# Optimization experiments

Hardware: AMD Instinct MI355X
Metric: run time of the kernel (lower is better)

Reference implementation:

```python
import jax, jax.numpy as jnp
import numpy as np

SHAPES = ((16, 16), (32, 32), (64, 64), (128, 128))  # (H, W) per level, low-res first
IN_CH = (2048, 1024, 512, 256)
B = 2; D = 256; HEADS = 4; PTS = 4; NLVL = 4; NLAYER = 3; DH = D // HEADS; FFN = 1024
LQ = sum(h * w for h, w in SHAPES)  # 21760


def _group_norm(x, g, b, groups=32, eps=1e-5):
    Bn, C, H, W = x.shape
    xr = x.reshape(Bn, groups, C // groups, H, W)
    m = xr.mean((2, 3, 4), keepdims=True)
    v = xr.var((2, 3, 4), keepdims=True)
    xr = (xr - m) / jnp.sqrt(v + eps)
    return xr.reshape(Bn, C, H, W) * g[None, :, None, None] + b[None, :, None, None]


def _layer_norm(x, g, b, eps=1e-5):
    m = x.mean(-1, keepdims=True)
    v = x.var(-1, keepdims=True)
    return (x - m) / jnp.sqrt(v + eps) * g + b


def _sine_pos(H, W):
    # PositionEmbeddingSine(num_pos_feats=D//2, normalize=True), mask all-valid
    nh = D // 2
    scale = 2.0 * np.pi
    dim_t = (10000.0 ** (2.0 * (jnp.arange(nh) // 2) / nh)).astype(jnp.float32)
    def enc(n, e):
        p = e[:, None] / dim_t  # (n, nh)
        return jnp.stack([jnp.sin(p[:, 0::2]), jnp.cos(p[:, 1::2])], -1).reshape(n, nh)
    ye = (jnp.arange(1, H + 1, dtype=jnp.float32) / (H + 1e-6)) * scale
    xe = (jnp.arange(1, W + 1, dtype=jnp.float32) / (W + 1e-6)) * scale
    py = enc(H, ye)  # (H, nh)
    px = enc(W, xe)  # (W, nh)
    pos = jnp.concatenate([jnp.broadcast_to(py[:, None], (H, W, nh)),
                           jnp.broadcast_to(px[None, :], (H, W, nh))], -1)
    return pos.reshape(H * W, D)


def _ref_points():
    refs = []
    for H, W in SHAPES:
        ry = (jnp.arange(H, dtype=jnp.float32) + 0.5) / H
        rx = (jnp.arange(W, dtype=jnp.float32) + 0.5) / W
        gy, gx = jnp.meshgrid(ry, rx, indexing='ij')
        refs.append(jnp.stack([gx.reshape(-1), gy.reshape(-1)], -1))
    return jnp.concatenate(refs, 0)  # (LQ, 2) in (x, y), identical across levels (valid_ratios==1)


def _bilinear(v, loc, H, W):
    # v: (B, HEADS, H*W, DH); loc: (B, LQ, HEADS, PTS, 2) normalized in [0,1]
    # grid_sample align_corners=False semantics: pixel = loc*size - 0.5, zero padding
    x = (loc[..., 0] * W - 0.5).transpose(0, 2, 1, 3)  # (B, HEADS, LQ, PTS)
    y = (loc[..., 1] * H - 0.5).transpose(0, 2, 1, 3)
    x0f = jnp.floor(x); y0f = jnp.floor(y)
    tx = x - x0f; ty = y - y0f
    x0 = x0f.astype(jnp.int32); y0 = y0f.astype(jnp.int32)
    def g(yi, xi):
        valid = ((xi >= 0) & (xi < W) & (yi >= 0) & (yi < H)).astype(v.dtype)
        idx = jnp.clip(yi, 0, H - 1) * W + jnp.clip(xi, 0, W - 1)
        out = jnp.take_along_axis(v, idx.reshape(B, HEADS, -1)[..., None], axis=2)
        return out.reshape(B, HEADS, LQ, PTS, DH) * valid[..., None]
    w00 = (1 - ty) * (1 - tx); w01 = (1 - ty) * tx
    w10 = ty * (1 - tx); w11 = ty * tx
    return (g(y0, x0) * w00[..., None] + g(y0, x0 + 1) * w01[..., None]
            + g(y0 + 1, x0) * w10[..., None] + g(y0 + 1, x0 + 1) * w11[..., None])


def _model(xs, pws, pbs, ggs, gbs, level_embed, Woff, boff, Wattn, battn,
           Wval, bval, Wout, bout, ng, nb, W1, b1, W2, b2):
    srcs, poss = [], []
    for i, ((H, W), x, pw, pb, gg, gb) in enumerate(zip(SHAPES, xs, pws, pbs, ggs, gbs)):
        z = jnp.einsum('bchw,dc->bdhw', x, pw) + pb[None, :, None, None]  # 1x1 conv
        z = _group_norm(z, gg, gb)
        srcs.append(z.reshape(B, D, H * W).transpose(0, 2, 1))  # (B, HW, D)
        poss.append(_sine_pos(H, W)[None] + level_embed[i][None, None])
    src = jnp.concatenate(srcs, 1)   # (B, LQ, D)
    pos = jnp.concatenate(poss, 1)   # (1, LQ, D)
    refs = _ref_points()             # (LQ, 2)
    wh = jnp.array([(W, H) for H, W in SHAPES], jnp.float32)  # (NLVL, 2) (x=W, y=H)
    for l in range(NLAYER):
        q = src + pos
        off = (q @ Woff[l] + boff[l]).reshape(B, LQ, HEADS, NLVL, PTS, 2)
        aw = jax.nn.softmax((q @ Wattn[l] + battn[l]).reshape(B, LQ, HEADS, NLVL * PTS), -1)
        aw = aw.reshape(B, LQ, HEADS, NLVL, PTS)
        val = (src @ Wval[l] + bval[l]).reshape(B, LQ, HEADS, DH)
        loc = refs[None, :, None, None, None, :] + off / wh[None, None, None, :, None, :]
        out = jnp.zeros((B, HEADS, LQ, DH), src.dtype)
        start = 0
        for lv, (H, W) in enumerate(SHAPES):
            n = H * W
            v = val[:, start:start + n].transpose(0, 2, 1, 3)        # (B, HEADS, n, DH)
            samp = _bilinear(v, loc[:, :, :, lv], H, W)              # (B, HEADS, LQ, PTS, DH)
            w = aw[:, :, :, lv].transpose(0, 2, 1, 3)                # (B, HEADS, LQ, PTS)
            out = out + jnp.einsum('bhqpd,bhqp->bhqd', samp, w)
            start += n
        attn_out = out.transpose(0, 2, 1, 3).reshape(B, LQ, D) @ Wout[l] + bout[l]
        src = _layer_norm(src + attn_out, ng[l], nb[l])
        # NOTE: per source, MLP output replaces src (no second residual)
        src = jax.nn.relu(src @ W1[l] + b1[l]) @ W2[l] + b2[l]
    return src


def setup_inputs():
    key = jax.random.key(0)
    ks = iter(jax.random.split(key, 24))
    inp = {}
    for i, (c, (H, W)) in enumerate(zip(IN_CH, SHAPES)):
        inp[f'x{i}'] = jax.random.normal(next(ks), (B, c, H, W), jnp.float32)
        inp[f'pw{i}'] = jax.random.normal(next(ks), (D, c), jnp.float32) / np.float32(np.sqrt(c))
        inp[f'pb{i}'] = jnp.zeros((D,), jnp.float32)
        inp[f'gg{i}'] = jnp.ones((D,), jnp.float32)
        inp[f'gb{i}'] = jnp.zeros((D,), jnp.float32)
    inp['level_embed'] = jax.random.normal(next(ks), (NLVL, D), jnp.float32)
    inp['Woff'] = jax.random.normal(next(ks), (NLAYER, D, HEADS * NLVL * PTS * 2), jnp.float32) * 0.01
    inp['boff'] = jax.random.normal(next(ks), (NLAYER, HEADS * NLVL * PTS * 2), jnp.float32) * 0.5
    inp['Wattn'] = jax.random.normal(next(ks), (NLAYER, D, HEADS * NLVL * PTS), jnp.float32) * 0.01
    inp['battn'] = jnp.zeros((NLAYER, HEADS * NLVL * PTS), jnp.float32)
    inp['Wval'] = jax.random.normal(next(ks), (NLAYER, D, D), jnp.float32) / 16.0
    inp['bval'] = jnp.zeros((NLAYER, D), jnp.float32)
    inp['Wout'] = jax.random.normal(next(ks), (NLAYER, D, D), jnp.float32) / 16.0
    inp['bout'] = jnp.zeros((NLAYER, D), jnp.float32)
    inp['ng'] = jnp.ones((NLAYER, D), jnp.float32)
    inp['nb'] = jnp.zeros((NLAYER, D), jnp.float32)
    inp['W1'] = jax.random.normal(next(ks), (NLAYER, D, FFN), jnp.float32) / 16.0
    inp['b1'] = jnp.zeros((NLAYER, FFN), jnp.float32)
    inp['W2'] = jax.random.normal(next(ks), (NLAYER, FFN, D), jnp.float32) / 32.0
    inp['b2'] = jnp.zeros((NLAYER, D), jnp.float32)
    return inp


def reference(x0, pw0, pb0, gg0, gb0, x1, pw1, pb1, gg1, gb1,
              x2, pw2, pb2, gg2, gb2, x3, pw3, pb3, gg3, gb3,
              level_embed, Woff, boff, Wattn, battn, Wval, bval, Wout, bout,
              ng, nb, W1, b1, W2, b2):
    return _model((x0, x1, x2, x3), (pw0, pw1, pw2, pw3), (pb0, pb1, pb2, pb3),
                  (gg0, gg1, gg2, gg3), (gb0, gb1, gb2, gb3), level_embed,
                  Woff, boff, Wattn, battn, Wval, bval, Wout, bout,
                  ng, nb, W1, b1, W2, b2)
```

## Files before the change

kernel.cpp:

```cpp
#include <hip/hip_runtime.h>
#include <math.h>

#define LQ 21760
#define NB 2

typedef __attribute__((ext_vector_type(8))) short bf16x8;
typedef __attribute__((ext_vector_type(4))) float f32x4;

static __device__ __forceinline__ float wave_sum(float v) {
#pragma unroll
    for (int o = 32; o > 0; o >>= 1) v += __shfl_down(v, o, 64);
    return v;
}

static __device__ __forceinline__ unsigned short f2bf(float f) {
    unsigned int u = __float_as_uint(f);
    u = (u + 0x7fffu + ((u >> 16) & 1u)) >> 16;
    return (unsigned short)u;
}
static __device__ __forceinline__ float bf2f(unsigned short h) {
    return __uint_as_float((unsigned int)h << 16);
}

__global__ __launch_bounds__(256) void zero_buf(float* __restrict__ p, int n) {
    const int i = blockIdx.x * 256 + threadIdx.x;
    if (i < n) p[i] = 0.f;
}

__global__ __launch_bounds__(256) void bias_cat(const float* __restrict__ boff,
                                                const float* __restrict__ battn,
                                                float* __restrict__ out) {
    const int idx = blockIdx.x * 256 + threadIdx.x;
    if (idx >= 3 * 192) return;
    const int l = idx / 192, i = idx - l * 192;
    out[idx] = (i < 128) ? boff[l * 128 + i] : battn[l * 64 + (i - 128)];
}

__global__ __launch_bounds__(256) void cvt_bf(const float* __restrict__ in,
                                              unsigned short* __restrict__ out, long n) {
    const long i = (long)blockIdx.x * 256 + threadIdx.x;
    if (i < n) out[i] = f2bf(in[i]);
}

__global__ __launch_bounds__(256) void transpose_cvt(const float* __restrict__ in,
                                                     unsigned short* __restrict__ out,
                                                     int Kr, int Nc)
{
    __shared__ float t[32][33];
    const int n0 = blockIdx.x * 32, k0 = blockIdx.y * 32;
    const int c = threadIdx.x & 31, r8 = threadIdx.x >> 5;
#pragma unroll
    for (int j = 0; j < 4; ++j) {
        const int r = r8 + j * 8;
        t[r][c] = in[(long)(k0 + r) * Nc + n0 + c];
    }
    __syncthreads();
#pragma unroll
    for (int j = 0; j < 4; ++j) {
        const int r = r8 + j * 8;
        out[(long)(n0 + r) * Kr + k0 + c] = f2bf(t[c][r]);
    }
}

__global__ __launch_bounds__(256) void transpose_cvt_x(const float* __restrict__ in,
                                                       unsigned short* __restrict__ out,
                                                       int C, int HW)
{
    __shared__ float t[32][33];
    const int hw0 = blockIdx.x * 32, c0 = blockIdx.y * 32;
    const int b = blockIdx.z;
    in  += (long)b * C * HW;
    out += (long)b * HW * C;
    const int cc = threadIdx.x & 31, rr = threadIdx.x >> 5;
#pragma unroll
    for (int j = 0; j < 4; ++j) {
        const int r = rr + j * 8;
        t[r][cc] = in[(long)(c0 + r) * HW + hw0 + cc];
    }
    __syncthreads();
#pragma unroll
    for (int j = 0; j < 4; ++j) {
        const int r = rr + j * 8;
        out[(long)(hw0 + r) * C + c0 + cc] = f2bf(t[cc][r]);
    }
}

template<int BN>
__global__ __launch_bounds__(256) void gemm_bf(
    const unsigned short* __restrict__ A, const unsigned short* __restrict__ Bt, int K,
    float* __restrict__ Cf, unsigned short* __restrict__ Cb, int ldc,
    const float* __restrict__ bias, int relu)
{
    constexpr int BM = 128, BK = 64, LDT = 72;
    __shared__ unsigned short As[BM * LDT];
    __shared__ unsigned short Bs[BN * LDT];
    const int tid = threadIdx.x;
    const long m0 = (long)blockIdx.y * BM;
    const int n0 = blockIdx.x * BN;
    const int wave = tid >> 6, lane = tid & 63;
    constexpr int WM = (BN == 128) ? 2 : 4;
    constexpr int FM = (BN == 128) ? 4 : 2;
    const int wm = wave % WM, wn = wave / WM;
    const int wm0 = wm * (BM / WM), wn0 = wn * 64;
    const int lrow = lane & 15, lk8 = (lane >> 4) * 8;
    f32x4 acc[FM][4] = {};
    for (int k0 = 0; k0 < K; k0 += BK) {
        __syncthreads();
        {
            const int r = tid >> 1, hh = (tid & 1) * 32;
            const unsigned short* ga = A + (m0 + r) * (long)K + k0 + hh;
            uint4 v0 = *(const uint4*)(ga);
            uint4 v1 = *(const uint4*)(ga + 8);
            uint4 v2 = *(const uint4*)(ga + 16);
            uint4 v3 = *(const uint4*)(ga + 24);
            unsigned short* la = &As[r * LDT + hh];
            *(uint4*)(la) = v0; *(uint4*)(la + 8) = v1;
            *(uint4*)(la + 16) = v2; *(uint4*)(la + 24) = v3;
        }
        if constexpr (BN == 128) {
            const int r = tid >> 1, hh = (tid & 1) * 32;
            const unsigned short* gb = Bt + (n0 + r) * (long)K + k0 + hh;
            uint4 v0 = *(const uint4*)(gb);
            uint4 v1 = *(const uint4*)(gb + 8);
            uint4 v2 = *(const uint4*)(gb + 16);
            uint4 v3 = *(const uint4*)(gb + 24);
            unsigned short* lb = &Bs[r * LDT + hh];
            *(uint4*)(lb) = v0; *(uint4*)(lb + 8) = v1;
            *(uint4*)(lb + 16) = v2; *(uint4*)(lb + 24) = v3;
        } else {
            const int r = tid >> 2, q8 = (tid & 3) * 16;
            const unsigned short* gb = Bt + (n0 + r) * (long)K + k0 + q8;
            uint4 v0 = *(const uint4*)(gb);
            uint4 v1 = *(const uint4*)(gb + 8);
            unsigned short* lb = &Bs[r * LDT + q8];
            *(uint4*)(lb) = v0; *(uint4*)(lb + 8) = v1;
        }
        __syncthreads();
        bf16x8 af[FM][2], bfr[4][2];
#pragma unroll
        for (int i = 0; i < FM; ++i)
#pragma unroll
            for (int kk = 0; kk < 2; ++kk)
                af[i][kk] = *(const bf16x8*)&As[(wm0 + i * 16 + lrow) * LDT + kk * 32 + lk8];
#pragma unroll
        for (int j = 0; j < 4; ++j)
#pragma unroll
            for (int kk = 0; kk < 2; ++kk)
                bfr[j][kk] = *(const bf16x8*)&Bs[(wn0 + j * 16 + lrow) * LDT + kk * 32 + lk8];
#pragma unroll
        for (int i = 0; i < FM; ++i)
#pragma unroll
            for (int j = 0; j < 4; ++j)
#pragma unroll
                for (int kk = 0; kk < 2; ++kk)
                    acc[i][j] = __builtin_amdgcn_mfma_f32_16x16x32_bf16(
                        af[i][kk], bfr[j][kk], acc[i][j], 0, 0, 0);
    }
    const int rbase = (lane >> 4) * 4;
#pragma unroll
    for (int i = 0; i < FM; ++i) {
#pragma unroll
        for (int j = 0; j < 4; ++j) {
            const int col = n0 + wn0 + j * 16 + lrow;
            const float bb = bias ? bias[col] : 0.f;
#pragma unroll
            for (int r = 0; r < 4; ++r) {
                float v = acc[i][j][r] + bb;
                if (relu) v = fmaxf(v, 0.f);
                const long row = m0 + wm0 + i * 16 + rbase + r;
                const long idx = row * (long)ldc + col;
                if (Cf) Cf[idx] = v;
                if (Cb) Cb[idx] = f2bf(v);
            }
        }
    }
}

__global__ __launch_bounds__(256) void pos_kernel(unsigned short* __restrict__ pos,
                                                  const float* __restrict__ lvl_emb)
{
    const int idx = blockIdx.x * 256 + threadIdx.x;
    const int d = idx & 255;
    const int i = idx >> 8;
    int lv, sz;
    if (i < 256)       { lv = 0; sz = 16; }
    else if (i < 1280) { lv = 1; sz = 32; }
    else if (i < 5376) { lv = 2; sz = 64; }
    else               { lv = 3; sz = 128; }
    const int base = (lv == 0) ? 0 : (lv == 1) ? 256 : (lv == 2) ? 1280 : 5376;
    const int hw = i - base;
    const int hy = hw / sz, wx = hw - hy * sz;
    const int dd = d & 127;
    const float twopi = 6.283185307179586f;
    const float e = ((d < 128) ? (float)(hy + 1) : (float)(wx + 1))
                    / ((float)sz + 1e-6f) * twopi;
    const float t = powf(10000.0f, (float)(2 * (dd >> 1)) * (1.0f / 128.0f));
    const float p = e / t;
    const float v = (dd & 1) ? cosf(p) : sinf(p);
    pos[idx] = f2bf(v + lvl_emb[lv * 256 + d]);
}

__global__ __launch_bounds__(256) void make_q2(const float* __restrict__ src,
                                               const unsigned short* __restrict__ pos,
                                               unsigned short* __restrict__ q, long total4)
{
    const long t = (long)blockIdx.x * 256 + threadIdx.x;
    if (t >= total4) return;
    const long idx = t * 4;
    const long pe = (idx >= (long)LQ * 256) ? idx - (long)LQ * 256 : idx;
    const float4 s = *(const float4*)(src + idx);
    const ushort4 pp = *(const ushort4*)(pos + pe);
    unsigned short o[4] = {f2bf(s.x + bf2f(pp.x)), f2bf(s.y + bf2f(pp.y)),
                           f2bf(s.z + bf2f(pp.z)), f2bf(s.w + bf2f(pp.w))};
    *(ushort4*)(q + idx) = *(const ushort4*)o;
}

__global__ __launch_bounds__(256) void gn_stats2(const float* __restrict__ z,
                                                 float* __restrict__ stats,
                                                 int HW, int span)
{
    const int b = blockIdx.y;
    const int hw0 = blockIdx.x * span;
    const int d = threadIdx.x;
    float s = 0.f, sq = 0.f;
    const float* p = z + ((long)b * HW + hw0) * 256 + d;
    for (int i = 0; i < span; ++i) {
        const float v = p[(long)i * 256];
        s += v; sq += v * v;
    }
#pragma unroll
    for (int o = 1; o < 8; o <<= 1) {
        s += __shfl_xor(s, o, 64);
        sq += __shfl_xor(sq, o, 64);
    }
    if ((d & 7) == 0) {
        atomicAdd(&stats[(b * 32 + (d >> 3)) * 2 + 0], s);
        atomicAdd(&stats[(b * 32 + (d >> 3)) * 2 + 1], sq);
    }
}

__global__ __launch_bounds__(256) void gn_scale(const float* __restrict__ z,
                                                float* __restrict__ src,
                                                unsigned short* __restrict__ src_bf,
                                                const float* __restrict__ stats,
                                                const float* __restrict__ gg,
                                                const float* __restrict__ gb,
                                                int hwShift, int lvl_base, long total4)
{
    const long t = (long)blockIdx.x * 256 + threadIdx.x;
    if (t >= total4) return;
    const int d4 = (int)(t & 63) * 4;
    const long row = t >> 6;
    const int b = (int)(row >> hwShift);
    const int hw = (int)(row & ((1 << hwShift) - 1));
    const int g = d4 >> 3;
    const float s = stats[(b * 32 + g) * 2 + 0];
    const float sq = stats[(b * 32 + g) * 2 + 1];
    const float cnt = 8.0f * (float)(1 << hwShift);
    const float m = s / cnt;
    const float rstd = rsqrtf(sq / cnt - m * m + 1e-5f);
    const float4 v = *(const float4*)(z + row * 256 + d4);
    float o[4];
    o[0] = (v.x - m) * rstd * gg[d4 + 0] + gb[d4 + 0];
    o[1] = (v.y - m) * rstd * gg[d4 + 1] + gb[d4 + 1];
    o[2] = (v.z - m) * rstd * gg[d4 + 2] + gb[d4 + 2];
    o[3] = (v.w - m) * rstd * gg[d4 + 3] + gb[d4 + 3];
    const long oidx = ((long)b * LQ + lvl_base + hw) * 256 + d4;
    *(float4*)(src + oidx) = make_float4(o[0], o[1], o[2], o[3]);
    unsigned short ob[4] = {f2bf(o[0]), f2bf(o[1]), f2bf(o[2]), f2bf(o[3])};
    *(ushort4*)(src_bf + oidx) = *(const ushort4*)ob;
}

__global__ __launch_bounds__(256) void softmax16_bf(unsigned short* __restrict__ oa, long total)
{
    const long t = (long)blockIdx.x * 256 + threadIdx.x;
    if (t >= total) return;
    unsigned short* p = oa + (t >> 2) * 192 + 128 + (t & 3) * 16;
    float v[16];
    float mx = -1e30f;
#pragma unroll
    for (int i = 0; i < 16; ++i) { v[i] = bf2f(p[i]); mx = fmaxf(mx, v[i]); }
    float s = 0.f;
#pragma unroll
    for (int i = 0; i < 16; ++i) { v[i] = __expf(v[i] - mx); s += v[i]; }
    const float inv = 1.0f / s;
#pragma unroll
    for (int i = 0; i < 16; ++i) p[i] = f2bf(v[i] * inv);
}

__global__ __launch_bounds__(256) void msda4(const unsigned short* __restrict__ val,
                                             const unsigned short* __restrict__ oa,
                                             unsigned short* __restrict__ out)
{
    const int bq = (blockIdx.x * 256 + threadIdx.x) >> 6;
    const int lane = threadIdx.x & 63;
    const int h = lane >> 4, c4 = (lane & 15) * 4;
    const int q = bq % LQ;
    const int b = bq / LQ;
    int Hq, bq0;
    if (q < 256)       { Hq = 16;  bq0 = 0; }
    else if (q < 1280) { Hq = 32;  bq0 = 256; }
    else if (q < 5376) { Hq = 64;  bq0 = 1280; }
    else               { Hq = 128; bq0 = 5376; }
    const int hw = q - bq0;
    const int qy = hw / Hq, qx = hw - qy * Hq;
    const float refx = ((float)qx + 0.5f) / (float)Hq;
    const float refy = ((float)qy + 0.5f) / (float)Hq;
    const unsigned short* oar = oa + (long)bq * 192;
    const int LH[4] = {16, 32, 64, 128};
    const int LB[4] = {0, 256, 1280, 5376};
    float ax = 0.f, ay = 0.f, az = 0.f, aw4 = 0.f;
#pragma unroll
    for (int lv = 0; lv < 4; ++lv) {
        const int Hl = LH[lv];
        const unsigned short* vb = val + ((long)b * LQ + LB[lv]) * 256 + h * 64 + c4;
#pragma unroll
        for (int p = 0; p < 4; ++p) {
            const unsigned int oxy = *(const unsigned int*)(oar + h * 32 + (lv * 4 + p) * 2);
            const float ox = bf2f((unsigned short)(oxy & 0xffffu));
            const float oy = bf2f((unsigned short)(oxy >> 16));
            const float w = bf2f(oar[128 + h * 16 + lv * 4 + p]);
            const float x = refx * (float)Hl + ox - 0.5f;
            const float y = refy * (float)Hl + oy - 0.5f;
            const float xf = floorf(x), yf = floorf(y);
            const float tx = x - xf, ty = y - yf;
            const int x0 = (int)xf, y0 = (int)yf;
            const float w00 = w * (1.f - ty) * (1.f - tx), w01 = w * (1.f - ty) * tx;
            const float w10 = w * ty * (1.f - tx),         w11 = w * ty * tx;
            const bool xv0 = (x0 >= 0) & (x0 < Hl);
            const bool xv1 = (x0 + 1 >= 0) & (x0 + 1 < Hl);
#define SAMPLE(WT, IDX) { const ushort4 vv = *(const ushort4*)(vb + (long)(IDX) * 256); \
        ax += (WT) * bf2f(vv.x); ay += (WT) * bf2f(vv.y); \
        az += (WT) * bf2f(vv.z); aw4 += (WT) * bf2f(vv.w); }
            if (y0 >= 0 && y0 < Hl) {
                const int r = y0 * Hl;
                if (xv0) SAMPLE(w00, r + x0)
                if (xv1) SAMPLE(w01, r + x0 + 1)
            }
            if (y0 + 1 >= 0 && y0 + 1 < Hl) {
                const int r = (y0 + 1) * Hl;
                if (xv0) SAMPLE(w10, r + x0)
                if (xv1) SAMPLE(w11, r + x0 + 1)
            }
#undef SAMPLE
        }
    }
    unsigned short o4[4] = {f2bf(ax), f2bf(ay), f2bf(az), f2bf(aw4)};
    *(ushort4*)(out + (long)bq * 256 + h * 64 + c4) = *(const ushort4*)o4;
}

__global__ __launch_bounds__(256) void ln_residual(const float* __restrict__ src,
                                                   const float* __restrict__ att,
                                                   unsigned short* __restrict__ outb,
                                                   const float* __restrict__ g,
                                                   const float* __restrict__ b)
{
    const long row = blockIdx.x;
    const int d = threadIdx.x;
    const long idx = row * 256 + d;
    const float v = src[idx] + att[idx];
    float s = wave_sum(v), sq = wave_sum(v * v);
    __shared__ float sh[8];
    const int wid = d >> 6, lane = d & 63;
    if (lane == 0) { sh[wid] = s; sh[4 + wid] = sq; }
    __syncthreads();
    const float S = sh[0] + sh[1] + sh[2] + sh[3];
    const float SQ = sh[4] + sh[5] + sh[6] + sh[7];
    const float m = S * (1.0f / 256.0f);
    const float var = SQ * (1.0f / 256.0f) - m * m;
    const float r = rsqrtf(var + 1e-5f);
    outb[idx] = f2bf((v - m) * r * g[d] + b[d]);
}

extern "C" void kernel_launch(void* const* d_in, const int* in_sizes, int n_in,
                              void* d_out, int out_size, void* d_ws, size_t ws_size,
                              hipStream_t stream)
{
    const float* x[4]  = {(const float*)d_in[0],  (const float*)d_in[5],
                          (const float*)d_in[10], (const float*)d_in[15]};
    const float* pw[4] = {(const float*)d_in[1],  (const float*)d_in[6],
                          (const float*)d_in[11], (const float*)d_in[16]};
    const float* pb[4] = {(const float*)d_in[2],  (const float*)d_in[7],
                          (const float*)d_in[12], (const float*)d_in[17]};
    const float* gg[4] = {(const float*)d_in[3],  (const float*)d_in[8],
                          (const float*)d_in[13], (const float*)d_in[18]};
    const float* gb[4] = {(const float*)d_in[4],  (const float*)d_in[9],
                          (const float*)d_in[14], (const float*)d_in[19]};
    const float* lvl_emb = (const float*)d_in[20];
    const float* Woff  = (const float*)d_in[21];
    const float* boff  = (const float*)d_in[22];
    const float* Wattn = (const float*)d_in[23];
    const float* battn = (const float*)d_in[24];
    const float* Wval  = (const float*)d_in[25];
    const float* bval  = (const float*)d_in[26];
    const float* Wout  = (const float*)d_in[27];
    const float* bout  = (const float*)d_in[28];
    const float* ng    = (const float*)d_in[29];
    const float* nbb   = (const float*)d_in[30];
    const float* W1    = (const float*)d_in[31];
    const float* b1    = (const float*)d_in[32];
    const float* W2    = (const float*)d_in[33];
    const float* b2    = (const float*)d_in[34];

    const long M = (long)NB * LQ;
    const long SRC_F    = 0;
    const long SRCBF_F  = 11141120;
    const long SHARED_F = SRCBF_F + 5570560;
    const long OA_F     = SHARED_F + 5570560;
    const long POS_F    = OA_F + 4177920;
    const long WT_F     = POS_F + 2785280;
    const long BIAS_F   = WT_F + 1056768;
    const long STATS_F  = BIAS_F + 576;
    const long NEED_F   = STATS_F + 512;
    if (ws_size < (size_t)NEED_F * sizeof(float)) return;

    float* ws = (float*)d_ws;
    float*          src    = ws + SRC_F;
    unsigned short* src_bf = (unsigned short*)(ws + SRCBF_F);
    unsigned short* shbf   = (unsigned short*)(ws + SHARED_F);
    unsigned short* oab    = (unsigned short*)(ws + OA_F);
    unsigned short* posbf  = (unsigned short*)(ws + POS_F);
    unsigned short* wT     = (unsigned short*)(ws + WT_F);
    float*          biasoa = ws + BIAS_F;
    float*          stats  = ws + STATS_F;
    float*          zbuf   = ws + SHARED_F;
    unsigned short* pwbf   = (unsigned short*)(ws + SHARED_F + 8388608);
    float*          Bbuf   = (float*)d_out;

    const long OAT = 0;
    const long VALT = OAT + 3 * 49152;
    const long OUTT = VALT + 3 * 65536;
    const long W1T = OUTT + 3 * 65536;
    const long W2T = W1T + 3 * 262144;

    zero_buf<<<2, 256, 0, stream>>>(stats, 512);
    bias_cat<<<3, 256, 0, stream>>>(boff, battn, biasoa);
    pos_kernel<<<LQ, 256, 0, stream>>>(posbf, lvl_emb);
    for (int l = 0; l < 3; ++l) {
        transpose_cvt<<<dim3(4, 8),  256, 0, stream>>>(Woff + (long)l * 32768,  wT + OAT + l * 49152, 256, 128);
        transpose_cvt<<<dim3(2, 8),  256, 0, stream>>>(Wattn + (long)l * 16384, wT + OAT + l * 49152 + 128 * 256, 256, 64);
        transpose_cvt<<<dim3(8, 8),  256, 0, stream>>>(Wval + (long)l * 65536,  wT + VALT + l * 65536, 256, 256);
        transpose_cvt<<<dim3(8, 8),  256, 0, stream>>>(Wout + (long)l * 65536,  wT + OUTT + l * 65536, 256, 256);
        transpose_cvt<<<dim3(32, 8), 256, 0, stream>>>(W1 + (long)l * 262144,   wT + W1T + l * 262144, 256, 1024);
        transpose_cvt<<<dim3(8, 32), 256, 0, stream>>>(W2 + (long)l * 262144,   wT + W2T + l * 262144, 1024, 256);
    }

    const int LC[4] = {2048, 1024, 512, 256};
    long pwoff[4];
    {
        long o = 0;
        for (int lv = 0; lv < 4; ++lv) { pwoff[lv] = o; o += (long)LC[lv] * 256; }
    }
    for (int lv = 0; lv < 4; ++lv)
        cvt_bf<<<(int)((LC[lv] * 256 + 255) / 256), 256, 0, stream>>>(
            pw[lv], pwbf + pwoff[lv], (long)LC[lv] * 256);

    const int LHW[4]   = {256, 1024, 4096, 16384};
    const int LSH[4]   = {8, 10, 12, 14};
    const int LBASE[4] = {0, 256, 1280, 5376};
    for (int lv = 0; lv < 4; ++lv) {
        const int HW = LHW[lv], C = LC[lv];
        transpose_cvt_x<<<dim3(HW / 32, C / 32, NB), 256, 0, stream>>>(
            x[lv], (unsigned short*)Bbuf, C, HW);
        gemm_bf<128><<<dim3(2, NB * HW / 128), 256, 0, stream>>>(
            (const unsigned short*)Bbuf, pwbf + pwoff[lv], C,
            zbuf, nullptr, 256, pb[lv], 0);
        gn_stats2<<<dim3(HW / 64, NB), 256, 0, stream>>>(zbuf, stats + lv * 128, HW, 64);
        const long total4 = (long)NB * HW * 64;
        gn_scale<<<(int)((total4 + 255) / 256), 256, 0, stream>>>(
            zbuf, src, src_bf, stats + lv * 128, gg[lv], gb[lv],
            LSH[lv], LBASE[lv], total4);
    }

    for (int l = 0; l < 3; ++l) {
        make_q2<<<10880, 256, 0, stream>>>(src, posbf, shbf, M * 64);
        gemm_bf<64><<<dim3(3, 340), 256, 0, stream>>>(
            shbf, wT + OAT + (long)l * 49152, 256, nullptr, oab, 192,
            biasoa + l * 192, 0);
        softmax16_bf<<<680, 256, 0, stream>>>(oab, M * 4);
        gemm_bf<128><<<dim3(2, 340), 256, 0, stream>>>(
            src_bf, wT + VALT + (long)l * 65536, 256, nullptr, (unsigned short*)Bbuf, 256,
            bval + l * 256, 0);
        msda4<<<10880, 256, 0, stream>>>((const unsigned short*)Bbuf, oab, shbf);
        gemm_bf<128><<<dim3(2, 340), 256, 0, stream>>>(
            shbf, wT + OUTT + (long)l * 65536, 256, Bbuf, nullptr, 256,
            bout + l * 256, 0);
        ln_residual<<<(int)M, 256, 0, stream>>>(src, Bbuf, shbf, ng + l * 256, nbb + l * 256);
        unsigned short* hid = (l < 2) ? (unsigned short*)d_out : (unsigned short*)src;
        for (int hf = 0; hf < 2; ++hf) {
            const long r0 = (long)hf * (M / 2);
            gemm_bf<128><<<dim3(8, 170), 256, 0, stream>>>(
                shbf + r0 * 256, wT + W1T + (long)l * 262144, 256,
                nullptr, hid, 1024, b1 + l * 1024, 1);
            float* cf = ((l < 2) ? src : (float*)d_out) + r0 * 256;
            unsigned short* cb = (l < 2) ? (src_bf + r0 * 256) : nullptr;
            gemm_bf<128><<<dim3(2, 170), 256, 0, stream>>>(
                hid, wT + W2T + (long)l * 262144, 1024,
                cf, cb, 256, b2 + l * 256, 0);
        }
    }
}
```

Measured before the change: 1.624 ms.

## Use direct global-to-LDS loads with XOR swizzle in GEMM; widen MSDA sampling to 8 channels

Measured after the change: 1.376 ms. 1.18x faster.

```diff
diff --git a/kernel.cpp b/kernel.cpp
--- a/kernel.cpp
+++ b/kernel.cpp
@@ -20,6 +20,18 @@
 }
 static __device__ __forceinline__ float bf2f(unsigned short h) {
     return __uint_as_float((unsigned int)h << 16);
+}
+static __device__ __forceinline__ float bflo(unsigned int u) {
+    return __uint_as_float(u << 16);
+}
+static __device__ __forceinline__ float bfhi(unsigned int u) {
+    return __uint_as_float(u & 0xffff0000u);
+}
+
+static __device__ __forceinline__ void gload16(const void* g, void* l) {
+    __builtin_amdgcn_global_load_lds(
+        (const __attribute__((address_space(1))) unsigned int*)g,
+        (__attribute__((address_space(3))) unsigned int*)l, 16, 0, 0);
 }
 
 __global__ __launch_bounds__(256) void zero_buf(float* __restrict__ p, int n) {
@@ -91,9 +103,10 @@
     float* __restrict__ Cf, unsigned short* __restrict__ Cb, int ldc,
     const float* __restrict__ bias, int relu)
 {
-    constexpr int BM = 128, BK = 64, LDT = 72;
-    __shared__ unsigned short As[BM * LDT];
-    __shared__ unsigned short Bs[BN * LDT];
+    constexpr int BM = 128, BK = 64;
+    constexpr int BINST = (BN == 128) ? 4 : 2;
+    __shared__ unsigned short As[BM * BK];
+    __shared__ unsigned short Bs[BN * BK];
     const int tid = threadIdx.x;
     const long m0 = (long)blockIdx.y * BM;
     const int n0 = blockIdx.x * BN;
@@ -103,50 +116,51 @@
     const int wm = wave % WM, wn = wave / WM;
     const int wm0 = wm * (BM / WM), wn0 = wn * 64;
     const int lrow = lane & 15, lk8 = (lane >> 4) * 8;
+    const int axor = (lrow & 7) << 4;
     f32x4 acc[FM][4] = {};
+    int arow[4], acolb[4], brow[BINST], bcolb[BINST];
+#pragma unroll
+    for (int j = 0; j < 4; ++j) {
+        const int p = (wave * 4 + j) * 1024 + lane * 16;
+        const int r = p >> 7;
+        arow[j] = r;
+        acolb[j] = (p & 127) ^ ((r & 7) << 4);
+    }
+#pragma unroll
+    for (int j = 0; j < BINST; ++j) {
+        const int p = (wave * BINST + j) * 1024 + lane * 16;
+        const int r = p >> 7;
+        brow[j] = r;
+        bcolb[j] = (p & 127) ^ ((r & 7) << 4);
+    }
     for (int k0 = 0; k0 < K; k0 += BK) {
         __syncthreads();
-        {
-            const int r = tid >> 1, hh = (tid & 1) * 32;
-            const unsigned short* ga = A + (m0 + r) * (long)K + k0 + hh;
-            uint4 v0 = *(const uint4*)(ga);
-            uint4 v1 = *(const uint4*)(ga + 8);
-            uint4 v2 = *(const uint4*)(ga + 16);
-            uint4 v3 = *(const uint4*)(ga + 24);
-            unsigned short* la = &As[r * LDT + hh];
-            *(uint4*)(la) = v0; *(uint4*)(la + 8) = v1;
-            *(uint4*)(la + 16) = v2; *(uint4*)(la + 24) = v3;
-        }
-        if constexpr (BN == 128) {
-            const int r = tid >> 1, hh = (tid & 1) * 32;
-            const unsigned short* gb = Bt + (n0 + r) * (long)K + k0 + hh;
-            uint4 v0 = *(const uint4*)(gb);
-            uint4 v1 = *(const uint4*)(gb + 8);
-            uint4 v2 = *(const uint4*)(gb + 16);
-            uint4 v3 = *(const uint4*)(gb + 24);
-            unsigned short* lb = &Bs[r * LDT + hh];
-            *(uint4*)(lb) = v0; *(uint4*)(lb + 8) = v1;
-            *(uint4*)(lb + 16) = v2; *(uint4*)(lb + 24) = v3;
-        } else {
-            const int r = tid >> 2, q8 = (tid & 3) * 16;
-            const unsigned short* gb = Bt + (n0 + r) * (long)K + k0 + q8;
-            uint4 v0 = *(const uint4*)(gb);
-            uint4 v1 = *(const uint4*)(gb + 8);
-            unsigned short* lb = &Bs[r * LDT + q8];
-            *(uint4*)(lb) = v0; *(uint4*)(lb + 8) = v1;
-        }
+#pragma unroll
+        for (int j = 0; j < 4; ++j)
+            gload16(A + (m0 + arow[j]) * (long)K + k0 + (acolb[j] >> 1),
+                    (char*)As + (wave * 4 + j) * 1024 + lane * 16);
+#pragma unroll
+        for (int j = 0; j < BINST; ++j)
+            gload16(Bt + (long)(n0 + brow[j]) * K + k0 + (bcolb[j] >> 1),
+                    (char*)Bs + (wave * BINST + j) * 1024 + lane * 16);
         __syncthreads();
         bf16x8 af[FM][2], bfr[4][2];
 #pragma unroll
         for (int i = 0; i < FM; ++i)
 #pragma unroll
-            for (int kk = 0; kk < 2; ++kk)
-                af[i][kk] = *(const bf16x8*)&As[(wm0 + i * 16 + lrow) * LDT + kk * 32 + lk8];
+            for (int kk = 0; kk < 2; ++kk) {
+                const int row = wm0 + i * 16 + lrow;
+                const int cb = ((kk * 32 + lk8) << 1) ^ axor;
+                af[i][kk] = *(const bf16x8*)((const char*)As + (row << 7) + cb);
+            }
 #pragma unroll
         for (int j = 0; j < 4; ++j)
 #pragma unroll
-            for (int kk = 0; kk < 2; ++kk)
-                bfr[j][kk] = *(const bf16x8*)&Bs[(wn0 + j * 16 + lrow) * LDT + kk * 32 + lk8];
+            for (int kk = 0; kk < 2; ++kk) {
+                const int row = wn0 + j * 16 + lrow;
+                const int cb = ((kk * 32 + lk8) << 1) ^ axor;
+                bfr[j][kk] = *(const bf16x8*)((const char*)Bs + (row << 7) + cb);
+            }
 #pragma unroll
         for (int i = 0; i < FM; ++i)
 #pragma unroll
@@ -288,13 +302,15 @@
     for (int i = 0; i < 16; ++i) p[i] = f2bf(v[i] * inv);
 }
 
-__global__ __launch_bounds__(256) void msda4(const unsigned short* __restrict__ val,
+__global__ __launch_bounds__(256) void msda8(const unsigned short* __restrict__ val,
                                              const unsigned short* __restrict__ oa,
                                              unsigned short* __restrict__ out)
 {
-    const int bq = (blockIdx.x * 256 + threadIdx.x) >> 6;
+    const int w = (blockIdx.x * 256 + threadIdx.x) >> 6;
     const int lane = threadIdx.x & 63;
-    const int h = lane >> 4, c4 = (lane & 15) * 4;
+    const int bq = w * 2 + (lane >> 5);
+    const int h = (lane >> 3) & 3;
+    const int c8 = (lane & 7) * 8;
     const int q = bq % LQ;
     const int b = bq / LQ;
     int Hq, bq0;
@@ -309,29 +325,32 @@
     const unsigned short* oar = oa + (long)bq * 192;
     const int LH[4] = {16, 32, 64, 128};
     const int LB[4] = {0, 256, 1280, 5376};
-    float ax = 0.f, ay = 0.f, az = 0.f, aw4 = 0.f;
+    float a0 = 0.f, a1 = 0.f, a2 = 0.f, a3 = 0.f;
+    float a4 = 0.f, a5 = 0.f, a6 = 0.f, a7 = 0.f;
 #pragma unroll
     for (int lv = 0; lv < 4; ++lv) {
         const int Hl = LH[lv];
-        const unsigned short* vb = val + ((long)b * LQ + LB[lv]) * 256 + h * 64 + c4;
+        const unsigned short* vb = val + ((long)b * LQ + LB[lv]) * 256 + h * 64 + c8;
 #pragma unroll
         for (int p = 0; p < 4; ++p) {
             const unsigned int oxy = *(const unsigned int*)(oar + h * 32 + (lv * 4 + p) * 2);
             const float ox = bf2f((unsigned short)(oxy & 0xffffu));
             const float oy = bf2f((unsigned short)(oxy >> 16));
-            const float w = bf2f(oar[128 + h * 16 + lv * 4 + p]);
+            const float wgt = bf2f(oar[128 + h * 16 + lv * 4 + p]);
             const float x = refx * (float)Hl + ox - 0.5f;
             const float y = refy * (float)Hl + oy - 0.5f;
             const float xf = floorf(x), yf = floorf(y);
             const float tx = x - xf, ty = y - yf;
             const int x0 = (int)xf, y0 = (int)yf;
-            const float w00 = w * (1.f - ty) * (1.f - tx), w01 = w * (1.f - ty) * tx;
-            const float w10 = w * ty * (1.f - tx),         w11 = w * ty * tx;
+            const float w00 = wgt * (1.f - ty) * (1.f - tx), w01 = wgt * (1.f - ty) * tx;
+            const float w10 = wgt * ty * (1.f - tx),         w11 = wgt * ty * tx;
             const bool xv0 = (x0 >= 0) & (x0 < Hl);
             const bool xv1 = (x0 + 1 >= 0) & (x0 + 1 < Hl);
-#define SAMPLE(WT, IDX) { const ushort4 vv = *(const ushort4*)(vb + (long)(IDX) * 256); \
-        ax += (WT) * bf2f(vv.x); ay += (WT) * bf2f(vv.y); \
-        az += (WT) * bf2f(vv.z); aw4 += (WT) * bf2f(vv.w); }
+#define SAMPLE(WT, IDX) { const uint4 vv = *(const uint4*)(vb + (long)(IDX) * 256); \
+        a0 += (WT) * bflo(vv.x); a1 += (WT) * bfhi(vv.x); \
+        a2 += (WT) * bflo(vv.y); a3 += (WT) * bfhi(vv.y); \
+        a4 += (WT) * bflo(vv.z); a5 += (WT) * bfhi(vv.z); \
+        a6 += (WT) * bflo(vv.w); a7 += (WT) * bfhi(vv.w); }
             if (y0 >= 0 && y0 < Hl) {
                 const int r = y0 * Hl;
                 if (xv0) SAMPLE(w00, r + x0)
@@ -345,8 +364,12 @@
 #undef SAMPLE
         }
     }
-    unsigned short o4[4] = {f2bf(ax), f2bf(ay), f2bf(az), f2bf(aw4)};
-    *(ushort4*)(out + (long)bq * 256 + h * 64 + c4) = *(const ushort4*)o4;
+    unsigned int r0 = (unsigned int)f2bf(a0) | ((unsigned int)f2bf(a1) << 16);
+    unsigned int r1 = (unsigned int)f2bf(a2) | ((unsigned int)f2bf(a3) << 16);
+    unsigned int r2 = (unsigned int)f2bf(a4) | ((unsigned int)f2bf(a5) << 16);
+    unsigned int r3 = (unsigned int)f2bf(a6) | ((unsigned int)f2bf(a7) << 16);
+    uint4 o = make_uint4(r0, r1, r2, r3);
+    *(uint4*)(out + (long)bq * 256 + h * 64 + c8) = o;
 }
 
 __global__ __launch_bounds__(256) void ln_residual(const float* __restrict__ src,
@@ -481,7 +504,7 @@
         gemm_bf<128><<<dim3(2, 340), 256, 0, stream>>>(
             src_bf, wT + VALT + (long)l * 65536, 256, nullptr, (unsigned short*)Bbuf, 256,
             bval + l * 256, 0);
-        msda4<<<10880, 256, 0, stream>>>((const unsigned short*)Bbuf, oab, shbf);
+        msda8<<<5440, 256, 0, stream>>>((const unsigned short*)Bbuf, oab, shbf);
         gemm_bf<128><<<dim3(2, 340), 256, 0, stream>>>(
             shbf, wT + OUTT + (long)l * 65536, 256, Bbuf, nullptr, 256,
             bout + l * 256, 0);
```
